# Kernel tuning notes

Measured on AMD Instinct MI355X. Metric: run time of the kernel, lower is better.

## Reference

```python
import jax, jax.numpy as jnp
import numpy as np

MAX_DISP = 192

def _conv(x, w, b=None, stride=1, pad=0):
    y = jax.lax.conv_general_dilated(x, w, (stride, stride), [(pad, pad), (pad, pad)],
                                     dimension_numbers=('NCHW', 'OIHW', 'NCHW'))
    return y if b is None else y + b[None, :, None, None]

def _inorm(x):  # InstanceNorm2d, affine=False
    m = x.mean((2, 3), keepdims=True)
    v = x.var((2, 3), keepdims=True)
    return (x - m) * jax.lax.rsqrt(v + 1e-5)

def _bnorm(x):  # BatchNorm2d at init (gamma=1, beta=0), batch stats
    m = x.mean((0, 2, 3), keepdims=True)
    v = x.var((0, 2, 3), keepdims=True)
    return (x - m) * jax.lax.rsqrt(v + 1e-5)

def _encoder(x, w1, b1, w2, b2, w3, b3, norm):
    # simplified BasicEncoder: two stride-2 convs -> 1/4 resolution, then 1x1 proj
    x = jax.nn.relu(norm(_conv(x, w1, b1, 2, 3)))
    x = jax.nn.relu(norm(_conv(x, w2, b2, 2, 1)))
    return _conv(x, w3, b3, 1, 0)

def _forward(image1, image2, fnet_w1, fnet_b1, fnet_w2, fnet_b2, fnet_w3, fnet_b3,
             cnet_w1, cnet_b1, cnet_w2, cnet_b2, cnet_w3, cnet_b3,
             bform_a, bform_b, bform_cd_w, bform_cd_b,
             gru_wz, gru_bz, gru_wr, gru_br, gru_wq, gru_bq,
             disp_w1, disp_b1, disp_w2, disp_b2):
    i1 = 2.0 * (image1 / 255.0) - 1.0
    i2 = 2.0 * (image2 / 255.0) - 1.0
    fmap1 = _encoder(i1, fnet_w1, fnet_b1, fnet_w2, fnet_b2, fnet_w3, fnet_b3, _inorm)
    fmap2 = _encoder(i2, fnet_w1, fnet_b1, fnet_w2, fnet_b2, fnet_w3, fnet_b3, _inorm)
    hidden = jnp.tanh(_encoder(i1, cnet_w1, cnet_b1, cnet_w2, cnet_b2, cnet_w3, cnet_b3, _bnorm))
    Wf = fmap1.shape[3]
    for d in range(MAX_DISP // 4):  # 48 sequential width-sweep steps, shrinking overlap
        f1 = fmap1[:, :, :, d:]
        f2 = fmap2[:, :, :, :Wf - d] if d > 0 else fmap2
        # BilinearForm: a(x) + b(y) + cd(x*y), all 1x1 convs
        feat = _conv(f1, bform_a) + _conv(f2, bform_b) + _conv(f1 * f2, bform_cd_w, bform_cd_b)
        h = hidden[:, :, :, d:]
        # gru_input = cat(h, feat); ConvGRU cats hidden again -> [h, h, feat] = 96 ch
        hx = jnp.concatenate([h, h, feat], axis=1)
        z = jax.nn.sigmoid(_conv(hx, gru_wz, gru_bz, 1, 1))
        r = jax.nn.sigmoid(_conv(hx, gru_wr, gru_br, 1, 1))
        q = jnp.tanh(_conv(jnp.concatenate([r * h, h, feat], axis=1), gru_wq, gru_bq, 1, 1))
        h = (1.0 - z) * h + z * q
        hidden = hidden.at[:, :, :, d:].set(h)  # in-place scatter back
    # DisparityHead: conv3x3 -> relu -> conv3x3, negated
    return -_conv(jax.nn.relu(_conv(hidden, disp_w1, disp_b1, 1, 1)), disp_w2, disp_b2, 1, 1)

def setup_inputs():
    key = jax.random.key(0)
    ks = jax.random.split(key, 16)
    B, H, W, D = 1, 384, 640, 32
    def n(k, shape, scale=0.05):
        return (jax.random.normal(k, shape) * scale).astype(jnp.float32)
    z = lambda c: jnp.zeros((c,), jnp.float32)
    return {
        'image1': jax.random.uniform(ks[0], (B, 3, H, W), jnp.float32) * 255.0,
        'image2': jax.random.uniform(ks[1], (B, 3, H, W), jnp.float32) * 255.0,
        'fnet_w1': n(ks[2], (D, 3, 7, 7)), 'fnet_b1': z(D),
        'fnet_w2': n(ks[3], (D, D, 3, 3)), 'fnet_b2': z(D),
        'fnet_w3': n(ks[4], (D, D, 1, 1)), 'fnet_b3': z(D),
        'cnet_w1': n(ks[5], (D, 3, 7, 7)), 'cnet_b1': z(D),
        'cnet_w2': n(ks[6], (D, D, 3, 3)), 'cnet_b2': z(D),
        'cnet_w3': n(ks[7], (D, D, 1, 1)), 'cnet_b3': z(D),
        'bform_a': n(ks[8], (D, D, 1, 1)), 'bform_b': n(ks[9], (D, D, 1, 1)),
        'bform_cd_w': n(ks[10], (D, D, 1, 1)), 'bform_cd_b': z(D),
        'gru_wz': n(ks[11], (D, 3 * D, 3, 3)), 'gru_bz': z(D),
        'gru_wr': n(ks[12], (D, 3 * D, 3, 3)), 'gru_br': z(D),
        'gru_wq': n(ks[13], (D, 3 * D, 3, 3)), 'gru_bq': z(D),
        'disp_w1': n(ks[14], (64, D, 3, 3)), 'disp_b1': z(64),
        'disp_w2': n(ks[15], (1, 64, 3, 3)), 'disp_b2': z(1),
    }

def reference(image1, image2, fnet_w1, fnet_b1, fnet_w2, fnet_b2, fnet_w3, fnet_b3,
              cnet_w1, cnet_b1, cnet_w2, cnet_b2, cnet_w3, cnet_b3,
              bform_a, bform_b, bform_cd_w, bform_cd_b,
              gru_wz, gru_bz, gru_wr, gru_br, gru_wq, gru_bq,
              disp_w1, disp_b1, disp_w2, disp_b2):
    return _forward(image1, image2, fnet_w1, fnet_b1, fnet_w2, fnet_b2, fnet_w3, fnet_b3,
                    cnet_w1, cnet_b1, cnet_w2, cnet_b2, cnet_w3, cnet_b3,
                    bform_a, bform_b, bform_cd_w, bform_cd_b,
                    gru_wz, gru_bz, gru_wr, gru_br, gru_wq, gru_bq,
                    disp_w1, disp_b1, disp_w2, disp_b2)
```

## Files before the change

kernel.cpp:

```cpp
#include <hip/hip_runtime.h>
#include <math.h>

#define H0 384
#define W0 640
#define H1 192
#define W1 320
#define H2 96
#define W2 160
#define NP1 (H1*W1)
#define NP2 (H2*W2)
#define ND  48
#define NBLK2 (NP2/256)
#define CHW ((size_t)32*NP2)
#define PW 162
#define PH 98
#define PSL (PH*PW)
#define PCHW ((size_t)32*PSL)

typedef float v2f __attribute__((ext_vector_type(2)));


__global__ void zero_buf_kernel(float* __restrict__ p, size_t n) {
    size_t i = (size_t)blockIdx.x*256 + threadIdx.x;
    size_t stride = (size_t)gridDim.x*256;
    for (; i < n; i += stride) p[i] = 0.f;
}

__device__ __forceinline__ void twr_dev(const float* __restrict__ in, float* __restrict__ out,
                                        int idx, int CI, int K, int CO) {
    int co = idx % CO;
    int t  = idx / CO;
    int k  = t % K;
    int ci = t / K;
    out[idx] = in[(co*CI + ci)*K + k];
}

__global__ void prep_all(const float* __restrict__ fnet_w1, const float* __restrict__ cnet_w1,
                         const float* __restrict__ fnet_w2, const float* __restrict__ cnet_w2,
                         const float* __restrict__ fnet_w3, const float* __restrict__ cnet_w3,
                         const float* __restrict__ bform_a, const float* __restrict__ bform_b,
                         const float* __restrict__ bform_cd_w, const float* __restrict__ disp_w1,
                         const float* __restrict__ gru_wz, const float* __restrict__ gru_wr,
                         const float* __restrict__ gru_wq,
                         float* __restrict__ we1f, float* __restrict__ we1c,
                         float* __restrict__ we2f, float* __restrict__ we2c,
                         float* __restrict__ w3f, float* __restrict__ w3c,
                         float* __restrict__ wat, float* __restrict__ wbt,
                         float* __restrict__ wct, float* __restrict__ wd1t,
                         float4* __restrict__ wzrpk, float2* __restrict__ wqpk,
                         float* __restrict__ stats) {
    int i = blockIdx.x*256 + threadIdx.x;
    if (i < 4704) { twr_dev(fnet_w1, we1f, i, 3, 49, 32); return; }
    i -= 4704;
    if (i < 4704) { twr_dev(cnet_w1, we1c, i, 3, 49, 32); return; }
    i -= 4704;
    if (i < 9216) { twr_dev(fnet_w2, we2f, i, 32, 9, 32); return; }
    i -= 9216;
    if (i < 9216) { twr_dev(cnet_w2, we2c, i, 32, 9, 32); return; }
    i -= 9216;
    if (i < 1024) { twr_dev(fnet_w3, w3f, i, 32, 1, 32); return; }
    i -= 1024;
    if (i < 1024) { twr_dev(cnet_w3, w3c, i, 32, 1, 32); return; }
    i -= 1024;
    if (i < 1024) { twr_dev(bform_a, wat, i, 32, 1, 32); return; }
    i -= 1024;
    if (i < 1024) { twr_dev(bform_b, wbt, i, 32, 1, 32); return; }
    i -= 1024;
    if (i < 1024) { twr_dev(bform_cd_w, wct, i, 32, 1, 32); return; }
    i -= 1024;
    if (i < 18432) { twr_dev(disp_w1, wd1t, i, 32, 9, 64); return; }
    i -= 18432;
    if (i < 9216) {
        int k  = i % 9;
        int ci = (i/9) % 64;
        int cg = i / (9*64);
        int co0 = cg*2, co1 = co0 + 1;
        float z0, z1, r0, r1;
        if (ci < 32) {
            z0 = gru_wz[(co0*96 + ci)*9 + k] + gru_wz[(co0*96 + ci + 32)*9 + k];
            z1 = gru_wz[(co1*96 + ci)*9 + k] + gru_wz[(co1*96 + ci + 32)*9 + k];
            r0 = gru_wr[(co0*96 + ci)*9 + k] + gru_wr[(co0*96 + ci + 32)*9 + k];
            r1 = gru_wr[(co1*96 + ci)*9 + k] + gru_wr[(co1*96 + ci + 32)*9 + k];
        } else {
            z0 = gru_wz[(co0*96 + ci + 32)*9 + k];
            z1 = gru_wz[(co1*96 + ci + 32)*9 + k];
            r0 = gru_wr[(co0*96 + ci + 32)*9 + k];
            r1 = gru_wr[(co1*96 + ci + 32)*9 + k];
        }
        wzrpk[i] = make_float4(z0, z1, r0, r1);
        return;
    }
    i -= 9216;
    if (i < 13824) {
        int k  = i % 9;
        int ci = (i/9) % 96;
        int cg = i / (9*96);
        wqpk[i] = make_float2(gru_wq[((cg*2)*96 + ci)*9 + k], gru_wq[((cg*2+1)*96 + ci)*9 + k]);
        return;
    }
    i -= 13824;
    if (i < 384) stats[i] = 0.f;
}

__global__ void pad_init_kernel(const float* __restrict__ hidden, float* __restrict__ hwork) {
    int idx = blockIdx.x*256 + threadIdx.x;
    if (idx >= 32*PSL) return;
    int c = idx / PSL;
    int r = idx % PSL;
    int py = r / PW, px = r % PW;
    int y = py - 1, x = px - 1;
    float v = 0.f;
    if ((unsigned)y < (unsigned)H2 && (unsigned)x < (unsigned)W2)
        v = hidden[c*NP2 + y*W2 + x];
    hwork[idx] = v;
}


__global__ __launch_bounds__(256, 4)
void conv7s2_dual(const float* __restrict__ img,
                  const float* __restrict__ wtf, const float* __restrict__ wtc,
                  const float* __restrict__ bf, const float* __restrict__ bc,
                  float* __restrict__ outf, float* __restrict__ outc) {
    int co8 = blockIdx.y*8;
    int sp = blockIdx.x*256 + threadIdx.x;
    int oy = sp / W1, ox = sp % W1;
    float af[8], ac[8];
    #pragma unroll
    for (int j = 0; j < 8; ++j) { af[j] = bf[co8+j]; ac[j] = bc[co8+j]; }
    for (int ci = 0; ci < 3; ++ci) {
        for (int ky = 0; ky < 7; ++ky) {
            int iy = 2*oy - 3 + ky;
            if ((unsigned)iy >= (unsigned)H0) continue;
            const float* row  = img + ci*(H0*W0) + iy*W0;
            int wbase = (ci*49 + ky*7)*32 + co8;
            #pragma unroll
            for (int kx = 0; kx < 7; ++kx) {
                int ix = 2*ox - 3 + kx;
                if ((unsigned)ix >= (unsigned)W0) continue;
                float v = row[ix]*(2.0f/255.0f) - 1.0f;
                const float4* wpf = (const float4*)(wtf + wbase + kx*32);
                const float4* wpc = (const float4*)(wtc + wbase + kx*32);
                float4 f0 = wpf[0], f1 = wpf[1];
                float4 c0 = wpc[0], c1 = wpc[1];
                af[0] += v*f0.x; af[1] += v*f0.y; af[2] += v*f0.z; af[3] += v*f0.w;
                af[4] += v*f1.x; af[5] += v*f1.y; af[6] += v*f1.z; af[7] += v*f1.w;
                ac[0] += v*c0.x; ac[1] += v*c0.y; ac[2] += v*c0.z; ac[3] += v*c0.w;
                ac[4] += v*c1.x; ac[5] += v*c1.y; ac[6] += v*c1.z; ac[7] += v*c1.w;
            }
        }
    }
    #pragma unroll
    for (int j = 0; j < 8; ++j) {
        outf[(co8+j)*NP1 + sp] = af[j];
        outc[(co8+j)*NP1 + sp] = ac[j];
    }
}

__global__ void conv7s2_v3(const float* __restrict__ img, const float* __restrict__ wt,
                           const float* __restrict__ b, float* __restrict__ out) {
    int cg = blockIdx.y;
    int co16 = cg*16;
    int sp = blockIdx.x*256 + threadIdx.x;
    int oy = sp / W1, ox = sp % W1;
    float acc[16];
    #pragma unroll
    for (int j = 0; j < 16; ++j) acc[j] = b[co16+j];
    for (int ci = 0; ci < 3; ++ci) {
        for (int ky = 0; ky < 7; ++ky) {
            int iy = 2*oy - 3 + ky;
            if ((unsigned)iy >= (unsigned)H0) continue;
            const float* row  = img + ci*(H0*W0) + iy*W0;
            const float* wrow = wt + (ci*49 + ky*7)*32 + co16;
            #pragma unroll
            for (int kx = 0; kx < 7; ++kx) {
                int ix = 2*ox - 3 + kx;
                if ((unsigned)ix >= (unsigned)W0) continue;
                float v = row[ix]*(2.0f/255.0f) - 1.0f;
                const float4* wp = (const float4*)(wrow + kx*32);
                #pragma unroll
                for (int j4 = 0; j4 < 4; ++j4) {
                    float4 w4 = wp[j4];
                    acc[4*j4+0] += v*w4.x; acc[4*j4+1] += v*w4.y;
                    acc[4*j4+2] += v*w4.z; acc[4*j4+3] += v*w4.w;
                }
            }
        }
    }
    #pragma unroll
    for (int j = 0; j < 16; ++j) out[(co16+j)*NP1 + sp] = acc[j];
}

__global__ void stats_partial_kernel(const float* __restrict__ x, int N, float* __restrict__ st) {
    int c = blockIdx.x >> 3, sl = blockIdx.x & 7;
    int chunk = N >> 3;
    const float4* p = (const float4*)(x + (size_t)c*N + (size_t)sl*chunk);
    int n4 = chunk >> 2;
    float s = 0.f, s2 = 0.f;
    for (int i = threadIdx.x; i < n4; i += 256) {
        float4 v = p[i];
        s  += v.x + v.y + v.z + v.w;
        s2 += v.x*v.x + v.y*v.y + v.z*v.z + v.w*v.w;
    }
    __shared__ float sh1[256], sh2[256];
    sh1[threadIdx.x] = s; sh2[threadIdx.x] = s2;
    __syncthreads();
    for (int o = 128; o > 0; o >>= 1) {
        if (threadIdx.x < o) { sh1[threadIdx.x] += sh1[threadIdx.x+o]; sh2[threadIdx.x] += sh2[threadIdx.x+o]; }
        __syncthreads();
    }
    if (threadIdx.x == 0) { atomicAdd(&st[2*c], sh1[0]); atomicAdd(&st[2*c+1], sh2[0]); }
}

__global__ void conv3s2_fused(const float* __restrict__ in, const float* __restrict__ st,
                              const float* __restrict__ wt, const float* __restrict__ b,
                              float* __restrict__ out) {
    int cg = blockIdx.x / NBLK2;
    int sp = (blockIdx.x % NBLK2)*256 + threadIdx.x;
    int co8 = cg*8;
    int oy = sp / W2, ox = sp % W2;
    float acc[8];
    #pragma unroll
    for (int j = 0; j < 8; ++j) acc[j] = b[co8+j];
    for (int ci = 0; ci < 32; ++ci) {
        float m    = st[2*ci] * (1.0f/NP1);
        float var  = st[2*ci+1] * (1.0f/NP1) - m*m;
        float rstd = rsqrtf(var + 1e-5f);
        const float* ip  = in + ci*NP1;
        const float* wci = wt + ci*9*32 + co8;
        #pragma unroll
        for (int ky = 0; ky < 3; ++ky) {
            int iy = 2*oy - 1 + ky;
            if ((unsigned)iy >= (unsigned)H1) continue;
            const float* row = ip + iy*W1;
            #pragma unroll
            for (int kx = 0; kx < 3; ++kx) {
                int ix = 2*ox - 1 + kx;
                if ((unsigned)ix >= (unsigned)W1) continue;
                float t = fmaxf((row[ix] - m)*rstd, 0.f);
                const float4* wp = (const float4*)(wci + (ky*3+kx)*32);
                float4 w0 = wp[0], w1 = wp[1];
                acc[0] += t*w0.x; acc[1] += t*w0.y; acc[2] += t*w0.z; acc[3] += t*w0.w;
                acc[4] += t*w1.x; acc[5] += t*w1.y; acc[6] += t*w1.z; acc[7] += t*w1.w;
            }
        }
    }
    #pragma unroll
    for (int j = 0; j < 8; ++j) out[(co8+j)*NP2 + sp] = acc[j];
}

__global__ void conv1x1_fused(const float* __restrict__ in, const float* __restrict__ st,
                              const float* __restrict__ wt, const float* __restrict__ b,
                              float* __restrict__ out, int mode) {
    int cg = blockIdx.x / NBLK2;
    int sp = (blockIdx.x % NBLK2)*256 + threadIdx.x;
    int co8 = cg*8;
    float acc[8];
    #pragma unroll
    for (int j = 0; j < 8; ++j) acc[j] = b[co8+j];
    for (int ci = 0; ci < 32; ++ci) {
        float m    = st[2*ci] * (1.0f/NP2);
        float var  = st[2*ci+1] * (1.0f/NP2) - m*m;
        float rstd = rsqrtf(var + 1e-5f);
        float t = fmaxf((in[ci*NP2 + sp] - m)*rstd, 0.f);
        const float4* wp = (const float4*)(wt + ci*32 + co8);
        float4 w0 = wp[0], w1 = wp[1];
        acc[0] += t*w0.x; acc[1] += t*w0.y; acc[2] += t*w0.z; acc[3] += t*w0.w;
        acc[4] += t*w1.x; acc[5] += t*w1.y; acc[6] += t*w1.z; acc[7] += t*w1.w;
    }
    #pragma unroll
    for (int j = 0; j < 8; ++j) {
        float a = acc[j];
        if (mode) a = tanhf(a);
        out[(co8+j)*NP2 + sp] = a;
    }
}


__global__ void feat0_pad_kernel(const float* __restrict__ fmap1, const float* __restrict__ fmap2,
                                 const float* __restrict__ wat, const float* __restrict__ wbt,
                                 const float* __restrict__ wct, const float* __restrict__ bc,
                                 float* __restrict__ featA) {
    int cg  = blockIdx.x / NBLK2;
    int sp  = (blockIdx.x % NBLK2)*256 + threadIdx.x;
    int y = sp / W2;
    int gx = sp % W2;
    int co8 = cg*8;
    float acc[8];
    #pragma unroll
    for (int j = 0; j < 8; ++j) acc[j] = bc[co8+j];
    for (int ci = 0; ci < 32; ++ci) {
        float f1 = fmap1[ci*NP2 + sp];
        float f2 = fmap2[ci*NP2 + sp];
        float f12 = f1*f2;
        const float4* ap = (const float4*)(wat + ci*32 + co8);
        const float4* bp = (const float4*)(wbt + ci*32 + co8);
        const float4* cp = (const float4*)(wct + ci*32 + co8);
        float4 a0 = ap[0], a1 = ap[1];
        float4 b0 = bp[0], b1 = bp[1];
        float4 c0 = cp[0], c1 = cp[1];
        acc[0] += f1*a0.x + f2*b0.x + f12*c0.x;
        acc[1] += f1*a0.y + f2*b0.y + f12*c0.y;
        acc[2] += f1*a0.z + f2*b0.z + f12*c0.z;
        acc[3] += f1*a0.w + f2*b0.w + f12*c0.w;
        acc[4] += f1*a1.x + f2*b1.x + f12*c1.x;
        acc[5] += f1*a1.y + f2*b1.y + f12*c1.y;
        acc[6] += f1*a1.z + f2*b1.z + f12*c1.z;
        acc[7] += f1*a1.w + f2*b1.w + f12*c1.w;
    }
    float* dst = featA + (size_t)(y+1)*PW + (gx+1);
    #pragma unroll
    for (int j = 0; j < 8; ++j) dst[(size_t)(co8+j)*PSL] = acc[j];
}


__global__ __launch_bounds__(256, 4)
void zrq_a(const float* __restrict__ hworkA, const float* __restrict__ featA,
           const float* __restrict__ fmap1, const float* __restrict__ fmap2,
           const float4* __restrict__ wzrpk, const float2* __restrict__ wqpk,
           const float* __restrict__ wat, const float* __restrict__ wbt,
           const float* __restrict__ wct, const float* __restrict__ bfc,
           const float* __restrict__ bz, const float* __restrict__ br,
           float* __restrict__ zbuf, float* __restrict__ rhpad,
           float* __restrict__ featB, float* __restrict__ qpart,
           int d, int Wd) {
    __shared__ v2f lws[1152];
    __shared__ v2f lfa[32], lfb[32], lfc[32];
    int cg  = blockIdx.y >> 1;
    int job = blockIdx.y & 1;
    int co0 = cg*2;
    if (job == 0) {
        const float4* wsrc = wzrpk + (size_t)cg*576;
        for (int i = threadIdx.x; i < 576; i += 256) {
            float4 w = wsrc[i];
            lws[i]       = (v2f){w.x, w.y};
            lws[576 + i] = (v2f){w.z, w.w};
        }
    } else {
        const float2* wsrc = wqpk + (size_t)cg*864 + 288;
        for (int i = threadIdx.x; i < 576; i += 256) {
            float2 w = wsrc[i];
            lws[i] = (v2f){w.x, w.y};
        }
        if (threadIdx.x < 32) {
            int ci = threadIdx.x;
            lfa[ci] = (v2f){wat[ci*32+co0], wat[ci*32+co0+1]};
            lfb[ci] = (v2f){wbt[ci*32+co0], wbt[ci*32+co0+1]};
            lfc[ci] = (v2f){wct[ci*32+co0], wct[ci*32+co0+1]};
        }
    }
    __syncthreads();
    int sp2 = blockIdx.x*256 + threadIdx.x;
    if (sp2 >= 48*Wd) return;
    int rp = sp2 / Wd;
    int lx = sp2 - rp*Wd;
    int y0 = rp*2;
    int gx = d + lx;
    size_t poff = (size_t)(y0+1)*PW + (gx+1);
    int ub = y0*W2 + gx;

    if (job == 0) {
        if (lx == 0) {
            #pragma unroll
            for (int j = 0; j < 2; ++j) {
                rhpad[(size_t)(co0+j)*PSL + poff - 1]      = 0.f;
                rhpad[(size_t)(co0+j)*PSL + poff + PW - 1] = 0.f;
            }
        }
        v2f az0 = (v2f){bz[co0], bz[co0+1]}, az1 = az0;
        v2f ar0 = (v2f){br[co0], br[co0+1]}, ar1 = ar0;
        #pragma unroll
        for (int pass = 0; pass < 2; ++pass) {
            const float* p = (pass == 0 ? hworkA : featA) + poff;
            const v2f* wz = lws + pass*288;
            const v2f* wr = lws + 576 + pass*288;
            #pragma unroll 2
            for (int ci = 0; ci < 32; ++ci) {
                float v[12];
                #pragma unroll
                for (int r = 0; r < 4; ++r) {
                    v[r*3+0] = p[(r-1)*PW - 1];
                    v[r*3+1] = p[(r-1)*PW    ];
                    v[r*3+2] = p[(r-1)*PW + 1];
                }
                #pragma unroll
                for (int k = 0; k < 9; ++k) {
                    int ky = k/3, kx = k - 3*ky;
                    float t0 = v[ky*3+kx];
                    float t1 = v[(ky+1)*3+kx];
                    v2f wzk = wz[k], wrk = wr[k];
                    az0 += wzk*(v2f){t0,t0}; az1 += wzk*(v2f){t1,t1};
                    ar0 += wrk*(v2f){t0,t0}; ar1 += wrk*(v2f){t1,t1};
                }
                p += PSL;
                wz += 9; wr += 9;
            }
        }
        v2f z0, z1, r0, r1;
        z0.x = 1.f/(1.f + __expf(-az0.x)); z0.y = 1.f/(1.f + __expf(-az0.y));
        z1.x = 1.f/(1.f + __expf(-az1.x)); z1.y = 1.f/(1.f + __expf(-az1.y));
        r0.x = 1.f/(1.f + __expf(-ar0.x)); r0.y = 1.f/(1.f + __expf(-ar0.y));
        r1.x = 1.f/(1.f + __expf(-ar1.x)); r1.y = 1.f/(1.f + __expf(-ar1.y));
        float h00 = hworkA[(size_t)co0*PSL + poff];
        float h01 = hworkA[(size_t)(co0+1)*PSL + poff];
        float h10 = hworkA[(size_t)co0*PSL + poff + PW];
        float h11 = hworkA[(size_t)(co0+1)*PSL + poff + PW];
        zbuf[(size_t)co0*NP2 + ub]          = z0.x;
        zbuf[(size_t)(co0+1)*NP2 + ub]      = z0.y;
        zbuf[(size_t)co0*NP2 + ub + W2]     = z1.x;
        zbuf[(size_t)(co0+1)*NP2 + ub + W2] = z1.y;
        rhpad[(size_t)co0*PSL + poff]          = r0.x*h00;
        rhpad[(size_t)(co0+1)*PSL + poff]      = r0.y*h01;
        rhpad[(size_t)co0*PSL + poff + PW]     = r1.x*h10;
        rhpad[(size_t)(co0+1)*PSL + poff + PW] = r1.y*h11;
    } else {
        int dn = d + 1;
        if (dn < ND) {
            if (lx == 0) {
                #pragma unroll
                for (int j = 0; j < 2; ++j) {
                    featB[(size_t)(co0+j)*PSL + poff]      = 0.f;
                    featB[(size_t)(co0+j)*PSL + poff + PW] = 0.f;
                }
            } else {
                v2f f0 = (v2f){bfc[co0], bfc[co0+1]};
                v2f f1 = f0;
                int base1 = y0*W2 + gx;
                #pragma unroll 2
                for (int ci = 0; ci < 32; ++ci) {
                    float a1 = fmap1[ci*NP2 + base1];
                    float a2 = fmap1[ci*NP2 + base1 + W2];
                    float b1 = fmap2[ci*NP2 + base1 - dn];
                    float b2 = fmap2[ci*NP2 + base1 + W2 - dn];
                    v2f wa = lfa[ci], wb = lfb[ci], wc = lfc[ci];
                    f0 += wa*(v2f){a1,a1} + wb*(v2f){b1,b1} + wc*(v2f){a1*b1,a1*b1};
                    f1 += wa*(v2f){a2,a2} + wb*(v2f){b2,b2} + wc*(v2f){a2*b2,a2*b2};
                }
                featB[(size_t)co0*PSL + poff]          = f0.x;
                featB[(size_t)(co0+1)*PSL + poff]      = f0.y;
                featB[(size_t)co0*PSL + poff + PW]     = f1.x;
                featB[(size_t)(co0+1)*PSL + poff + PW] = f1.y;
            }
        }
        v2f a0 = (v2f){0.f, 0.f};
        v2f a1 = a0;
        #pragma unroll
        for (int pass = 0; pass < 2; ++pass) {
            const float* p = (pass == 0 ? hworkA : featA) + poff;
            const v2f* wp = lws + pass*288;
            #pragma unroll 2
            for (int ci = 0; ci < 32; ++ci) {
                float v[12];
                #pragma unroll
                for (int r = 0; r < 4; ++r) {
                    v[r*3+0] = p[(r-1)*PW - 1];
                    v[r*3+1] = p[(r-1)*PW    ];
                    v[r*3+2] = p[(r-1)*PW + 1];
                }
                #pragma unroll
                for (int k = 0; k < 9; ++k) {
                    int ky = k/3, kx = k - 3*ky;
                    float t0 = v[ky*3+kx];
                    float t1 = v[(ky+1)*3+kx];
                    v2f wk = wp[k];
                    a0 += wk*(v2f){t0,t0};
                    a1 += wk*(v2f){t1,t1};
                }
                p += PSL;
                wp += 9;
            }
        }
        qpart[(size_t)co0*NP2 + ub]          = a0.x;
        qpart[(size_t)(co0+1)*NP2 + ub]      = a0.y;
        qpart[(size_t)co0*NP2 + ub + W2]     = a1.x;
        qpart[(size_t)(co0+1)*NP2 + ub + W2] = a1.y;
    }
}

__global__ __launch_bounds__(256, 4)
void q_fin(const float* __restrict__ rhpad, const float* __restrict__ hworkA,
           const float* __restrict__ zbuf, const float* __restrict__ qpart,
           const float2* __restrict__ wqpk, const float* __restrict__ bq,
           float* __restrict__ hfinal, float* __restrict__ hworkB, int d, int Wd) {
    __shared__ v2f lw[288];
    int cg  = blockIdx.y;
    int co0 = cg*2;
    {
        const float2* wsrc = wqpk + (size_t)cg*864;
        for (int i = threadIdx.x; i < 288; i += 256) {
            float2 w = wsrc[i];
            lw[i] = (v2f){w.x, w.y};
        }
    }
    __syncthreads();
    int sp2 = blockIdx.x*256 + threadIdx.x;
    if (sp2 >= 48*Wd) return;
    int rp = sp2 / Wd;
    int lx = sp2 - rp*Wd;
    int y0 = rp*2;
    int gx = d + lx;
    size_t poff = (size_t)(y0+1)*PW + (gx+1);
    int ub = y0*W2 + gx;

    v2f a0 = (v2f){bq[co0], bq[co0+1]};
    v2f a1 = a0;
    {
        const float* p = rhpad + poff;
        const v2f* wp = lw;
        #pragma unroll 2
        for (int ci = 0; ci < 32; ++ci) {
            float v[12];
            #pragma unroll
            for (int r = 0; r < 4; ++r) {
                v[r*3+0] = p[(r-1)*PW - 1];
                v[r*3+1] = p[(r-1)*PW    ];
                v[r*3+2] = p[(r-1)*PW + 1];
            }
            #pragma unroll
            for (int k = 0; k < 9; ++k) {
                int ky = k/3, kx = k - 3*ky;
                float t0 = v[ky*3+kx];
                float t1 = v[(ky+1)*3+kx];
                v2f wk = wp[k];
                a0 += wk*(v2f){t0,t0};
                a1 += wk*(v2f){t1,t1};
            }
            p += PSL;
            wp += 9;
        }
    }
    a0.x += qpart[(size_t)co0*NP2 + ub];
    a0.y += qpart[(size_t)(co0+1)*NP2 + ub];
    a1.x += qpart[(size_t)co0*NP2 + ub + W2];
    a1.y += qpart[(size_t)(co0+1)*NP2 + ub + W2];
    float q00 = tanhf(a0.x), q01 = tanhf(a0.y);
    float q10 = tanhf(a1.x), q11 = tanhf(a1.y);
    #pragma unroll
    for (int j = 0; j < 2; ++j) {
        float qa = (j == 0) ? q00 : q01;
        float qb = (j == 0) ? q10 : q11;
        size_t pidx = (size_t)(co0+j)*PSL + poff;
        size_t uidx = (size_t)(co0+j)*NP2 + ub;
        float z_a = zbuf[uidx];
        float z_b = zbuf[uidx + W2];
        float h_a = hworkA[pidx];
        float h_b = hworkA[pidx + PW];
        float hn_a = (1.f - z_a)*h_a + z_a*qa;
        float hn_b = (1.f - z_b)*h_b + z_b*qb;
        if (lx == 0 || d == ND-1) {
            hfinal[pidx]      = hn_a;
            hfinal[pidx + PW] = hn_b;
        }
        hworkB[pidx]      = (lx == 0) ? 0.f : hn_a;
        hworkB[pidx + PW] = (lx == 0) ? 0.f : hn_b;
    }
}


__global__ __launch_bounds__(256, 4)
void disp1_v6(const float* __restrict__ hfinal, const float* __restrict__ wt,
              const float* __restrict__ b, float* __restrict__ out) {
    __shared__ float4 lw[288];
    int cg  = blockIdx.y;
    int co0 = cg*4;
    for (int i = threadIdx.x; i < 288; i += 256)
        lw[i] = *(const float4*)&wt[i*64 + co0];
    __syncthreads();
    int sp2 = blockIdx.x*256 + threadIdx.x;
    int y0 = (sp2 / W2)*2;
    int gx = sp2 % W2;
    size_t poff = (size_t)(y0+1)*PW + (gx+1);
    float4 bb = *(const float4*)&b[co0];
    float acc0[4] = {bb.x, bb.y, bb.z, bb.w};
    float acc1[4] = {bb.x, bb.y, bb.z, bb.w};
    const float* p = hfinal + poff;
    #pragma unroll 2
    for (int ci = 0; ci < 32; ++ci) {
        float v[12];
        #pragma unroll
        for (int r = 0; r < 4; ++r) {
            v[r*3+0] = p[(r-1)*PW - 1];
            v[r*3+1] = p[(r-1)*PW    ];
            v[r*3+2] = p[(r-1)*PW + 1];
        }
        #pragma unroll
        for (int k = 0; k < 9; ++k) {
            int ky = k/3, kx = k - 3*ky;
            float t0 = v[ky*3+kx];
            float t1 = v[(ky+1)*3+kx];
            float4 w = lw[ci*9+k];
            acc0[0] += t0*w.x; acc0[1] += t0*w.y; acc0[2] += t0*w.z; acc0[3] += t0*w.w;
            acc1[0] += t1*w.x; acc1[1] += t1*w.y; acc1[2] += t1*w.z; acc1[3] += t1*w.w;
        }
        p += PSL;
    }
    int ub = y0*W2 + gx;
    #pragma unroll
    for (int j = 0; j < 4; ++j) {
        out[(co0+j)*NP2 + ub]      = fmaxf(acc0[j], 0.f);
        out[(co0+j)*NP2 + ub + W2] = fmaxf(acc1[j], 0.f);
    }
}

__global__ void disp2_part_kernel(const float* __restrict__ in, const float* __restrict__ w,
                                  float* __restrict__ part) {
    __shared__ float lw[8*9];
    int g  = blockIdx.x / NBLK2;
    int sp = (blockIdx.x % NBLK2)*256 + threadIdx.x;
    if (threadIdx.x < 72) lw[threadIdx.x] = w[g*72 + threadIdx.x];
    __syncthreads();
    int y = sp / W2, x = sp % W2;
    float acc = 0.f;
    #pragma unroll
    for (int ci = 0; ci < 8; ++ci) {
        const float* ip = in + (g*8 + ci)*NP2;
        #pragma unroll
        for (int dy = 0; dy < 3; ++dy) {
            int ys = y+dy-1; if ((unsigned)ys >= (unsigned)H2) continue;
            const float* row = ip + ys*W2;
            #pragma unroll
            for (int dx = 0; dx < 3; ++dx) {
                int xs = x+dx-1; if ((unsigned)xs >= (unsigned)W2) continue;
                acc += lw[ci*9+dy*3+dx] * row[xs];
            }
        }
    }
    part[g*NP2 + sp] = acc;
}

__global__ void disp2_comb_kernel(const float* __restrict__ part, const float* __restrict__ b,
                                  float* __restrict__ out) {
    int sp = blockIdx.x*256 + threadIdx.x;
    float acc = b[0];
    #pragma unroll
    for (int g = 0; g < 8; ++g) acc += part[g*NP2 + sp];
    out[sp] = -acc;
}


extern "C" void kernel_launch(void* const* d_in, const int* in_sizes, int n_in,
                              void* d_out, int out_size, void* d_ws, size_t ws_size,
                              hipStream_t stream) {
    const float* image1   = (const float*)d_in[0];
    const float* image2   = (const float*)d_in[1];
    const float* fnet_w1  = (const float*)d_in[2];
    const float* fnet_b1  = (const float*)d_in[3];
    const float* fnet_w2  = (const float*)d_in[4];
    const float* fnet_b2  = (const float*)d_in[5];
    const float* fnet_w3  = (const float*)d_in[6];
    const float* fnet_b3  = (const float*)d_in[7];
    const float* cnet_w1  = (const float*)d_in[8];
    const float* cnet_b1  = (const float*)d_in[9];
    const float* cnet_w2  = (const float*)d_in[10];
    const float* cnet_b2  = (const float*)d_in[11];
    const float* cnet_w3  = (const float*)d_in[12];
    const float* cnet_b3  = (const float*)d_in[13];
    const float* bform_a  = (const float*)d_in[14];
    const float* bform_b  = (const float*)d_in[15];
    const float* bform_cd_w = (const float*)d_in[16];
    const float* bform_cd_b = (const float*)d_in[17];
    const float* gru_wz   = (const float*)d_in[18];
    const float* gru_bz   = (const float*)d_in[19];
    const float* gru_wr   = (const float*)d_in[20];
    const float* gru_br   = (const float*)d_in[21];
    const float* gru_wq   = (const float*)d_in[22];
    const float* gru_bq   = (const float*)d_in[23];
    const float* disp_w1  = (const float*)d_in[24];
    const float* disp_b1  = (const float*)d_in[25];
    const float* disp_w2  = (const float*)d_in[26];
    const float* disp_b2  = (const float*)d_in[27];

    float* ws = (float*)d_ws;
    size_t o = 0;
    float* e1f    = ws + o; o += (size_t)32*NP1;
    float* e1c    = ws + o; o += (size_t)32*NP1;
    float* e2     = ws + o; o += CHW;
    float* fmap1  = ws + o; o += CHW;
    float* fmap2  = ws + o; o += CHW;
    float* hidden = ws + o; o += CHW;
    float* zbuf   = ws + o; o += CHW;
    float* qpart  = ws + o; o += CHW;
    float* hwork0 = ws + o; o += PCHW;
    float* hwork1 = ws + o; o += PCHW;
    float* rhpad  = ws + o; o += PCHW;
    float* feat0  = ws + o; o += PCHW;
    float* feat1  = ws + o; o += PCHW;
    float* hfinal = ws + o; o += PCHW;
    float* stats  = ws + o; o += 384;
    float* wzrpk  = ws + o; o += 16*64*9*4;
    float* wqpk   = ws + o; o += 16*96*9*2;
    float* we1f   = ws + o; o += 3*49*32;
    float* we1c   = ws + o; o += 3*49*32;
    float* we2f   = ws + o; o += 32*9*32;
    float* we2c   = ws + o; o += 32*9*32;
    float* w3f    = ws + o; o += 32*32;
    float* w3c    = ws + o; o += 32*32;
    float* wat    = ws + o; o += 32*32;
    float* wbt    = ws + o; o += 32*32;
    float* wct    = ws + o; o += 32*32;
    float* wd1t   = ws + o; o += 32*9*64;
    float* disp1buf  = e1f;
    float* disp2part = e1c;

    prep_all<<<(74816 + 255)/256, 256, 0, stream>>>(
        fnet_w1, cnet_w1, fnet_w2, cnet_w2, fnet_w3, cnet_w3,
        bform_a, bform_b, bform_cd_w, disp_w1, gru_wz, gru_wr, gru_wq,
        we1f, we1c, we2f, we2c, w3f, w3c, wat, wbt, wct, wd1t,
        (float4*)wzrpk, (float2*)wqpk, stats);

    conv7s2_dual<<<dim3(NP1/256, 4), 256, 0, stream>>>(image1, we1f, we1c, fnet_b1, cnet_b1,
                                                       e1f, e1c);
    stats_partial_kernel<<<256, 256, 0, stream>>>(e1f, NP1, stats+0);
    stats_partial_kernel<<<256, 256, 0, stream>>>(e1c, NP1, stats+64);
    conv3s2_fused<<<4*NBLK2, 256, 0, stream>>>(e1f, stats+0, we2f, fnet_b2, e2);
    stats_partial_kernel<<<256, 256, 0, stream>>>(e2, NP2, stats+128);
    conv1x1_fused<<<4*NBLK2, 256, 0, stream>>>(e2, stats+128, w3f, fnet_b3, fmap1, 0);
    conv3s2_fused<<<4*NBLK2, 256, 0, stream>>>(e1c, stats+64, we2c, cnet_b2, e2);
    stats_partial_kernel<<<256, 256, 0, stream>>>(e2, NP2, stats+192);
    conv1x1_fused<<<4*NBLK2, 256, 0, stream>>>(e2, stats+192, w3c, cnet_b3, hidden, 1);
    conv7s2_v3<<<dim3(NP1/256, 2), 256, 0, stream>>>(image2, we1f, fnet_b1, e1f);
    stats_partial_kernel<<<256, 256, 0, stream>>>(e1f, NP1, stats+256);
    conv3s2_fused<<<4*NBLK2, 256, 0, stream>>>(e1f, stats+256, we2f, fnet_b2, e2);
    stats_partial_kernel<<<256, 256, 0, stream>>>(e2, NP2, stats+320);
    conv1x1_fused<<<4*NBLK2, 256, 0, stream>>>(e2, stats+320, w3f, fnet_b3, fmap2, 0);

    zero_buf_kernel<<<2048, 256, 0, stream>>>(hwork1, 5*PCHW);
    pad_init_kernel<<<(32*PSL+255)/256, 256, 0, stream>>>(hidden, hwork0);
    feat0_pad_kernel<<<4*NBLK2, 256, 0, stream>>>(fmap1, fmap2, wat, wbt, wct,
                                                  bform_cd_b, feat0);

    float* hwA = hwork0; float* hwB = hwork1;
    float* ftA = feat0;  float* ftB = feat1;
    for (int d = 0; d < ND; ++d) {
        int Wd = W2 - d;
        int nblk = (48*Wd + 255)/256;
        zrq_a<<<dim3(nblk, 32), 256, 0, stream>>>(hwA, ftA, fmap1, fmap2,
                                                  (const float4*)wzrpk, (const float2*)wqpk,
                                                  wat, wbt, wct, bform_cd_b,
                                                  gru_bz, gru_br, zbuf, rhpad, ftB, qpart,
                                                  d, Wd);
        q_fin<<<dim3(nblk, 16), 256, 0, stream>>>(rhpad, hwA, zbuf, qpart,
                                                  (const float2*)wqpk, gru_bq,
                                                  hfinal, hwB, d, Wd);
        float* t;
        t = hwA; hwA = hwB; hwB = t;
        t = ftA; ftA = ftB; ftB = t;
    }

    disp1_v6<<<dim3(30, 16), 256, 0, stream>>>(hfinal, wd1t, disp_b1, disp1buf);
    disp2_part_kernel<<<8*NBLK2, 256, 0, stream>>>(disp1buf, disp_w2, disp2part);
    disp2_comb_kernel<<<NBLK2, 256, 0, stream>>>(disp2part, disp_b2, (float*)d_out);
}
```

Before: 2.681 ms.

## Fuse norm statistics into conv epilogues and split q-partial job across more blocks

Removes the separate stats_partial reduction kernels by having each conv kernel reduce its outputs per wavefront with shuffles and atomically add channel sum and sum-of-squares. It also splits the zrq_a q-partial work (hidden pass and feat pass) into two separate block jobs writing to two buffers, raising the grid from 32 to 48 y-blocks, and q_fin sums both partials. This trades extra atomics and an extra buffer read for fewer launches, less re-reading of activations, and more parallelism in the per-step loop. Atomic accumulation order changes floating-point summation order slightly.

Result: slower. 4.017 ms (+49.8%).

```diff
diff --git a/kernel.cpp b/kernel.cpp
--- a/kernel.cpp
+++ b/kernel.cpp
@@ -18,6 +18,24 @@
 #define PCHW ((size_t)32*PSL)
 
 typedef float v2f __attribute__((ext_vector_type(2)));
+
+__device__ __forceinline__ void wave_stats(float* __restrict__ st, int ch0,
+                                           const float* acc, int n) {
+    int lane = threadIdx.x & 63;
+    for (int j = 0; j < n; ++j) {
+        float s  = acc[j];
+        float s2 = s*s;
+        #pragma unroll
+        for (int off = 32; off > 0; off >>= 1) {
+            s  += __shfl_down(s,  off, 64);
+            s2 += __shfl_down(s2, off, 64);
+        }
+        if (lane == 0) {
+            atomicAdd(&st[2*(ch0+j)],   s);
+            atomicAdd(&st[2*(ch0+j)+1], s2);
+        }
+    }
+}
 
 
 __global__ void zero_buf_kernel(float* __restrict__ p, size_t n) {
@@ -120,7 +138,8 @@
 void conv7s2_dual(const float* __restrict__ img,
                   const float* __restrict__ wtf, const float* __restrict__ wtc,
                   const float* __restrict__ bf, const float* __restrict__ bc,
-                  float* __restrict__ outf, float* __restrict__ outc) {
+                  float* __restrict__ outf, float* __restrict__ outc,
+                  float* __restrict__ stf, float* __restrict__ stc) {
     int co8 = blockIdx.y*8;
     int sp = blockIdx.x*256 + threadIdx.x;
     int oy = sp / W1, ox = sp % W1;
@@ -154,10 +173,13 @@
         outf[(co8+j)*NP1 + sp] = af[j];
         outc[(co8+j)*NP1 + sp] = ac[j];
     }
+    wave_stats(stf, co8, af, 8);
+    wave_stats(stc, co8, ac, 8);
 }
 
 __global__ void conv7s2_v3(const float* __restrict__ img, const float* __restrict__ wt,
-                           const float* __restrict__ b, float* __restrict__ out) {
+                           const float* __restrict__ b, float* __restrict__ out,
+                           float* __restrict__ st) {
     int cg = blockIdx.y;
     int co16 = cg*16;
     int sp = blockIdx.x*256 + threadIdx.x;
@@ -188,32 +210,12 @@
     }
     #pragma unroll
     for (int j = 0; j < 16; ++j) out[(co16+j)*NP1 + sp] = acc[j];
-}
-
-__global__ void stats_partial_kernel(const float* __restrict__ x, int N, float* __restrict__ st) {
-    int c = blockIdx.x >> 3, sl = blockIdx.x & 7;
-    int chunk = N >> 3;
-    const float4* p = (const float4*)(x + (size_t)c*N + (size_t)sl*chunk);
-    int n4 = chunk >> 2;
-    float s = 0.f, s2 = 0.f;
-    for (int i = threadIdx.x; i < n4; i += 256) {
-        float4 v = p[i];
-        s  += v.x + v.y + v.z + v.w;
-        s2 += v.x*v.x + v.y*v.y + v.z*v.z + v.w*v.w;
-    }
-    __shared__ float sh1[256], sh2[256];
-    sh1[threadIdx.x] = s; sh2[threadIdx.x] = s2;
-    __syncthreads();
-    for (int o = 128; o > 0; o >>= 1) {
-        if (threadIdx.x < o) { sh1[threadIdx.x] += sh1[threadIdx.x+o]; sh2[threadIdx.x] += sh2[threadIdx.x+o]; }
-        __syncthreads();
-    }
-    if (threadIdx.x == 0) { atomicAdd(&st[2*c], sh1[0]); atomicAdd(&st[2*c+1], sh2[0]); }
+    wave_stats(st, co16, acc, 16);
 }
 
 __global__ void conv3s2_fused(const float* __restrict__ in, const float* __restrict__ st,
                               const float* __restrict__ wt, const float* __restrict__ b,
-                              float* __restrict__ out) {
+                              float* __restrict__ out, float* __restrict__ stout) {
     int cg = blockIdx.x / NBLK2;
     int sp = (blockIdx.x % NBLK2)*256 + threadIdx.x;
     int co8 = cg*8;
@@ -246,6 +248,7 @@
     }
     #pragma unroll
     for (int j = 0; j < 8; ++j) out[(co8+j)*NP2 + sp] = acc[j];
+    wave_stats(stout, co8, acc, 8);
 }
 
 __global__ void conv1x1_fused(const float* __restrict__ in, const float* __restrict__ st,
@@ -321,12 +324,12 @@
            const float* __restrict__ wct, const float* __restrict__ bfc,
            const float* __restrict__ bz, const float* __restrict__ br,
            float* __restrict__ zbuf, float* __restrict__ rhpad,
-           float* __restrict__ featB, float* __restrict__ qpart,
-           int d, int Wd) {
+           float* __restrict__ featB, float* __restrict__ qpartA,
+           float* __restrict__ qpartB, int d, int Wd) {
     __shared__ v2f lws[1152];
     __shared__ v2f lfa[32], lfb[32], lfc[32];
-    int cg  = blockIdx.y >> 1;
-    int job = blockIdx.y & 1;
+    int cg  = blockIdx.y / 3;
+    int job = blockIdx.y - cg*3;
     int co0 = cg*2;
     if (job == 0) {
         const float4* wsrc = wzrpk + (size_t)cg*576;
@@ -335,9 +338,9 @@
             lws[i]       = (v2f){w.x, w.y};
             lws[576 + i] = (v2f){w.z, w.w};
         }
-    } else {
+    } else if (job == 1) {
         const float2* wsrc = wqpk + (size_t)cg*864 + 288;
-        for (int i = threadIdx.x; i < 576; i += 256) {
+        for (int i = threadIdx.x; i < 288; i += 256) {
             float2 w = wsrc[i];
             lws[i] = (v2f){w.x, w.y};
         }
@@ -346,6 +349,12 @@
             lfa[ci] = (v2f){wat[ci*32+co0], wat[ci*32+co0+1]};
             lfb[ci] = (v2f){wbt[ci*32+co0], wbt[ci*32+co0+1]};
             lfc[ci] = (v2f){wct[ci*32+co0], wct[ci*32+co0+1]};
+        }
+    } else {
+        const float2* wsrc = wqpk + (size_t)cg*864 + 576;
+        for (int i = threadIdx.x; i < 288; i += 256) {
+            float2 w = wsrc[i];
+            lws[i] = (v2f){w.x, w.y};
         }
     }
     __syncthreads();
@@ -412,7 +421,7 @@
         rhpad[(size_t)(co0+1)*PSL + poff]      = r0.y*h01;
         rhpad[(size_t)co0*PSL + poff + PW]     = r1.x*h10;
         rhpad[(size_t)(co0+1)*PSL + poff + PW] = r1.y*h11;
-    } else {
+    } else if (job == 1) {
         int dn = d + 1;
         if (dn < ND) {
             if (lx == 0) {
@@ -443,10 +452,9 @@
         }
         v2f a0 = (v2f){0.f, 0.f};
         v2f a1 = a0;
-        #pragma unroll
-        for (int pass = 0; pass < 2; ++pass) {
-            const float* p = (pass == 0 ? hworkA : featA) + poff;
-            const v2f* wp = lws + pass*288;
+        {
+            const float* p = hworkA + poff;
+            const v2f* wp = lws;
             #pragma unroll 2
             for (int ci = 0; ci < 32; ++ci) {
                 float v[12];
@@ -469,16 +477,49 @@
                 wp += 9;
             }
         }
-        qpart[(size_t)co0*NP2 + ub]          = a0.x;
-        qpart[(size_t)(co0+1)*NP2 + ub]      = a0.y;
-        qpart[(size_t)co0*NP2 + ub + W2]     = a1.x;
-        qpart[(size_t)(co0+1)*NP2 + ub + W2] = a1.y;
+        qpartA[(size_t)co0*NP2 + ub]          = a0.x;
+        qpartA[(size_t)(co0+1)*NP2 + ub]      = a0.y;
+        qpartA[(size_t)co0*NP2 + ub + W2]     = a1.x;
+        qpartA[(size_t)(co0+1)*NP2 + ub + W2] = a1.y;
+    } else {
+        v2f a0 = (v2f){0.f, 0.f};
+        v2f a1 = a0;
+        {
+            const float* p = featA + poff;
+            const v2f* wp = lws;
+            #pragma unroll 2
+            for (int ci = 0; ci < 32; ++ci) {
+                float v[12];
+                #pragma unroll
+                for (int r = 0; r < 4; ++r) {
+                    v[r*3+0] = p[(r-1)*PW - 1];
+                    v[r*3+1] = p[(r-1)*PW    ];
+                    v[r*3+2] = p[(r-1)*PW + 1];
+                }
+                #pragma unroll
+                for (int k = 0; k < 9; ++k) {
+                    int ky = k/3, kx = k - 3*ky;
+                    float t0 = v[ky*3+kx];
+                    float t1 = v[(ky+1)*3+kx];
+                    v2f wk = wp[k];
+                    a0 += wk*(v2f){t0,t0};
+                    a1 += wk*(v2f){t1,t1};
+                }
+                p += PSL;
+                wp += 9;
+            }
+        }
+        qpartB[(size_t)co0*NP2 + ub]          = a0.x;
+        qpartB[(size_t)(co0+1)*NP2 + ub]      = a0.y;
+        qpartB[(size_t)co0*NP2 + ub + W2]     = a1.x;
+        qpartB[(size_t)(co0+1)*NP2 + ub + W2] = a1.y;
     }
 }
 
 __global__ __launch_bounds__(256, 4)
 void q_fin(const float* __restrict__ rhpad, const float* __restrict__ hworkA,
-           const float* __restrict__ zbuf, const float* __restrict__ qpart,
+           const float* __restrict__ zbuf, const float* __restrict__ qpartA,
+           const float* __restrict__ qpartB,
            const float2* __restrict__ wqpk, const float* __restrict__ bq,
            float* __restrict__ hfinal, float* __restrict__ hworkB, int d, int Wd) {
     __shared__ v2f lw[288];
@@ -520,7 +561,7 @@
                 int ky = k/3, kx = k - 3*ky;
                 float t0 = v[ky*3+kx];
                 float t1 = v[(ky+1)*3+kx];
-                v2f wk = wp[k];
+                v2f wk = lw[(wp - lw) + k];
                 a0 += wk*(v2f){t0,t0};
                 a1 += wk*(v2f){t1,t1};
             }
@@ -528,10 +569,10 @@
             wp += 9;
         }
     }
-    a0.x += qpart[(size_t)co0*NP2 + ub];
-    a0.y += qpart[(size_t)(co0+1)*NP2 + ub];
-    a1.x += qpart[(size_t)co0*NP2 + ub + W2];
-    a1.y += qpart[(size_t)(co0+1)*NP2 + ub + W2];
+    a0.x += qpartA[(size_t)co0*NP2 + ub]          + qpartB[(size_t)co0*NP2 + ub];
+    a0.y += qpartA[(size_t)(co0+1)*NP2 + ub]      + qpartB[(size_t)(co0+1)*NP2 + ub];
+    a1.x += qpartA[(size_t)co0*NP2 + ub + W2]     + qpartB[(size_t)co0*NP2 + ub + W2];
+    a1.y += qpartA[(size_t)(co0+1)*NP2 + ub + W2] + qpartB[(size_t)(co0+1)*NP2 + ub + W2];
     float q00 = tanhf(a0.x), q01 = tanhf(a0.y);
     float q10 = tanhf(a1.x), q11 = tanhf(a1.y);
     #pragma unroll
@@ -678,7 +719,8 @@
     float* fmap2  = ws + o; o += CHW;
     float* hidden = ws + o; o += CHW;
     float* zbuf   = ws + o; o += CHW;
-    float* qpart  = ws + o; o += CHW;
+    float* qpartA = ws + o; o += CHW;
+    float* qpartB = ws + o; o += CHW;
     float* hwork0 = ws + o; o += PCHW;
     float* hwork1 = ws + o; o += PCHW;
     float* rhpad  = ws + o; o += PCHW;
@@ -708,19 +750,13 @@
         (float4*)wzrpk, (float2*)wqpk, stats);
 
     conv7s2_dual<<<dim3(NP1/256, 4), 256, 0, stream>>>(image1, we1f, we1c, fnet_b1, cnet_b1,
-                                                       e1f, e1c);
-    stats_partial_kernel<<<256, 256, 0, stream>>>(e1f, NP1, stats+0);
-    stats_partial_kernel<<<256, 256, 0, stream>>>(e1c, NP1, stats+64);
-    conv3s2_fused<<<4*NBLK2, 256, 0, stream>>>(e1f, stats+0, we2f, fnet_b2, e2);
-    stats_partial_kernel<<<256, 256, 0, stream>>>(e2, NP2, stats+128);
+                                                       e1f, e1c, stats+0, stats+64);
+    conv3s2_fused<<<4*NBLK2, 256, 0, stream>>>(e1f, stats+0, we2f, fnet_b2, e2, stats+128);
     conv1x1_fused<<<4*NBLK2, 256, 0, stream>>>(e2, stats+128, w3f, fnet_b3, fmap1, 0);
-    conv3s2_fused<<<4*NBLK2, 256, 0, stream>>>(e1c, stats+64, we2c, cnet_b2, e2);
-    stats_partial_kernel<<<256, 256, 0, stream>>>(e2, NP2, stats+192);
+    conv3s2_fused<<<4*NBLK2, 256, 0, stream>>>(e1c, stats+64, we2c, cnet_b2, e2, stats+192);
     conv1x1_fused<<<4*NBLK2, 256, 0, stream>>>(e2, stats+192, w3c, cnet_b3, hidden, 1);
-    conv7s2_v3<<<dim3(NP1/256, 2), 256, 0, stream>>>(image2, we1f, fnet_b1, e1f);
-    stats_partial_kernel<<<256, 256, 0, stream>>>(e1f, NP1, stats+256);
-    conv3s2_fused<<<4*NBLK2, 256, 0, stream>>>(e1f, stats+256, we2f, fnet_b2, e2);
-    stats_partial_kernel<<<256, 256, 0, stream>>>(e2, NP2, stats+320);
+    conv7s2_v3<<<dim3(NP1/256, 2), 256, 0, stream>>>(image2, we1f, fnet_b1, e1f, stats+256);
+    conv3s2_fused<<<4*NBLK2, 256, 0, stream>>>(e1f, stats+256, we2f, fnet_b2, e2, stats+320);
     conv1x1_fused<<<4*NBLK2, 256, 0, stream>>>(e2, stats+320, w3f, fnet_b3, fmap2, 0);
 
     zero_buf_kernel<<<2048, 256, 0, stream>>>(hwork1, 5*PCHW);
@@ -733,12 +769,12 @@
     for (int d = 0; d < ND; ++d) {
         int Wd = W2 - d;
         int nblk = (48*Wd + 255)/256;
-        zrq_a<<<dim3(nblk, 32), 256, 0, stream>>>(hwA, ftA, fmap1, fmap2,
+        zrq_a<<<dim3(nblk, 48), 256, 0, stream>>>(hwA, ftA, fmap1, fmap2,
                                                   (const float4*)wzrpk, (const float2*)wqpk,
                                                   wat, wbt, wct, bform_cd_b,
-                                                  gru_bz, gru_br, zbuf, rhpad, ftB, qpart,
-                                                  d, Wd);
-        q_fin<<<dim3(nblk, 16), 256, 0, stream>>>(rhpad, hwA, zbuf, qpart,
+                                                  gru_bz, gru_br, zbuf, rhpad, ftB,
+                                                  qpartA, qpartB, d, Wd);
+        q_fin<<<dim3(nblk, 16), 256, 0, stream>>>(rhpad, hwA, zbuf, qpartA, qpartB,
                                                   (const float2*)wqpk, gru_bq,
                                                   hfinal, hwB, d, Wd);
         float* t;
```

## Batch the three encoder passes into single launches per stage

Applied to the files above, without the earlier changes.

Merges the fnet(image1), cnet(image1) and fnet(image2) encoder pipelines so that each stage (7x7 conv, stats, 3x3 conv, stats, 1x1 conv) runs as one grid that covers all three networks. This takes the encoder from 14 launches down to 5 and gives each launch more blocks, which should fill the GPU better during the small encoder stages. The 7x7 conv now uses 8 output channels per thread with launch_bounds raised to 8 blocks per SM. Separate intermediate buffers are allocated for each net, which uses more workspace. The encoder is probably a small share of the total time next to the 48-step GRU loop.

Result: faster. 2.554 ms (-4.7%).

```diff
diff --git a/kernel.cpp b/kernel.cpp
--- a/kernel.cpp
+++ b/kernel.cpp
@@ -116,81 +116,51 @@
 }
 
 
-__global__ __launch_bounds__(256, 4)
-void conv7s2_dual(const float* __restrict__ img,
-                  const float* __restrict__ wtf, const float* __restrict__ wtc,
-                  const float* __restrict__ bf, const float* __restrict__ bc,
-                  float* __restrict__ outf, float* __restrict__ outc) {
-    int co8 = blockIdx.y*8;
+__global__ __launch_bounds__(256, 8)
+void conv7s2_all(const float* __restrict__ img1, const float* __restrict__ img2,
+                 const float* __restrict__ wtf, const float* __restrict__ wtc,
+                 const float* __restrict__ bf, const float* __restrict__ bc,
+                 float* __restrict__ e1f, float* __restrict__ e1c, float* __restrict__ e1i2) {
+    int net = blockIdx.y >> 2;
+    int co8 = (blockIdx.y & 3)*8;
+    const float* img = (net == 2) ? img2 : img1;
+    const float* wt  = (net == 1) ? wtc : wtf;
+    const float* bb  = (net == 1) ? bc  : bf;
+    float* out = (net == 0) ? e1f : (net == 1 ? e1c : e1i2);
     int sp = blockIdx.x*256 + threadIdx.x;
     int oy = sp / W1, ox = sp % W1;
-    float af[8], ac[8];
-    #pragma unroll
-    for (int j = 0; j < 8; ++j) { af[j] = bf[co8+j]; ac[j] = bc[co8+j]; }
+    float acc[8];
+    #pragma unroll
+    for (int j = 0; j < 8; ++j) acc[j] = bb[co8+j];
     for (int ci = 0; ci < 3; ++ci) {
         for (int ky = 0; ky < 7; ++ky) {
             int iy = 2*oy - 3 + ky;
             if ((unsigned)iy >= (unsigned)H0) continue;
             const float* row  = img + ci*(H0*W0) + iy*W0;
-            int wbase = (ci*49 + ky*7)*32 + co8;
-            #pragma unroll
-            for (int kx = 0; kx < 7; ++kx) {
-                int ix = 2*ox - 3 + kx;
-                if ((unsigned)ix >= (unsigned)W0) continue;
-                float v = row[ix]*(2.0f/255.0f) - 1.0f;
-                const float4* wpf = (const float4*)(wtf + wbase + kx*32);
-                const float4* wpc = (const float4*)(wtc + wbase + kx*32);
-                float4 f0 = wpf[0], f1 = wpf[1];
-                float4 c0 = wpc[0], c1 = wpc[1];
-                af[0] += v*f0.x; af[1] += v*f0.y; af[2] += v*f0.z; af[3] += v*f0.w;
-                af[4] += v*f1.x; af[5] += v*f1.y; af[6] += v*f1.z; af[7] += v*f1.w;
-                ac[0] += v*c0.x; ac[1] += v*c0.y; ac[2] += v*c0.z; ac[3] += v*c0.w;
-                ac[4] += v*c1.x; ac[5] += v*c1.y; ac[6] += v*c1.z; ac[7] += v*c1.w;
-            }
-        }
-    }
-    #pragma unroll
-    for (int j = 0; j < 8; ++j) {
-        outf[(co8+j)*NP1 + sp] = af[j];
-        outc[(co8+j)*NP1 + sp] = ac[j];
-    }
-}
-
-__global__ void conv7s2_v3(const float* __restrict__ img, const float* __restrict__ wt,
-                           const float* __restrict__ b, float* __restrict__ out) {
-    int cg = blockIdx.y;
-    int co16 = cg*16;
-    int sp = blockIdx.x*256 + threadIdx.x;
-    int oy = sp / W1, ox = sp % W1;
-    float acc[16];
-    #pragma unroll
-    for (int j = 0; j < 16; ++j) acc[j] = b[co16+j];
-    for (int ci = 0; ci < 3; ++ci) {
-        for (int ky = 0; ky < 7; ++ky) {
-            int iy = 2*oy - 3 + ky;
-            if ((unsigned)iy >= (unsigned)H0) continue;
-            const float* row  = img + ci*(H0*W0) + iy*W0;
-            const float* wrow = wt + (ci*49 + ky*7)*32 + co16;
+            const float* wrow = wt + (ci*49 + ky*7)*32 + co8;
             #pragma unroll
             for (int kx = 0; kx < 7; ++kx) {
                 int ix = 2*ox - 3 + kx;
                 if ((unsigned)ix >= (unsigned)W0) continue;
                 float v = row[ix]*(2.0f/255.0f) - 1.0f;
                 const float4* wp = (const float4*)(wrow + kx*32);
-                #pragma unroll
-                for (int j4 = 0; j4 < 4; ++j4) {
-                    float4 w4 = wp[j4];
-                    acc[4*j4+0] += v*w4.x; acc[4*j4+1] += v*w4.y;
-                    acc[4*j4+2] += v*w4.z; acc[4*j4+3] += v*w4.w;
-                }
-            }
-        }
-    }
-    #pragma unroll
-    for (int j = 0; j < 16; ++j) out[(co16+j)*NP1 + sp] = acc[j];
-}
-
-__global__ void stats_partial_kernel(const float* __restrict__ x, int N, float* __restrict__ st) {
+                float4 w0 = wp[0], w1 = wp[1];
+                acc[0] += v*w0.x; acc[1] += v*w0.y; acc[2] += v*w0.z; acc[3] += v*w0.w;
+                acc[4] += v*w1.x; acc[5] += v*w1.y; acc[6] += v*w1.z; acc[7] += v*w1.w;
+            }
+        }
+    }
+    #pragma unroll
+    for (int j = 0; j < 8; ++j) out[(co8+j)*NP1 + sp] = acc[j];
+}
+
+__global__ void stats3_kernel(const float* __restrict__ b0, const float* __restrict__ b1,
+                              const float* __restrict__ b2, int N,
+                              float* __restrict__ st0, float* __restrict__ st1,
+                              float* __restrict__ st2) {
+    int job = blockIdx.y;
+    const float* x = (job == 0) ? b0 : (job == 1 ? b1 : b2);
+    float* st      = (job == 0) ? st0 : (job == 1 ? st1 : st2);
     int c = blockIdx.x >> 3, sl = blockIdx.x & 7;
     int chunk = N >> 3;
     const float4* p = (const float4*)(x + (size_t)c*N + (size_t)sl*chunk);
@@ -211,12 +181,20 @@
     if (threadIdx.x == 0) { atomicAdd(&st[2*c], sh1[0]); atomicAdd(&st[2*c+1], sh2[0]); }
 }
 
-__global__ void conv3s2_fused(const float* __restrict__ in, const float* __restrict__ st,
-                              const float* __restrict__ wt, const float* __restrict__ b,
-                              float* __restrict__ out) {
-    int cg = blockIdx.x / NBLK2;
-    int sp = (blockIdx.x % NBLK2)*256 + threadIdx.x;
-    int co8 = cg*8;
+__global__ void conv3s2_all(const float* __restrict__ e1f, const float* __restrict__ e1c,
+                            const float* __restrict__ e1i2, const float* __restrict__ stats,
+                            const float* __restrict__ we2f, const float* __restrict__ we2c,
+                            const float* __restrict__ fb2, const float* __restrict__ cb2,
+                            float* __restrict__ e2f, float* __restrict__ e2c,
+                            float* __restrict__ e2i2) {
+    int net = blockIdx.y >> 2;
+    int co8 = (blockIdx.y & 3)*8;
+    const float* in = (net == 0) ? e1f : (net == 1 ? e1c : e1i2);
+    const float* st = (net == 0) ? stats+0 : (net == 1 ? stats+64 : stats+256);
+    const float* wt = (net == 1) ? we2c : we2f;
+    const float* b  = (net == 1) ? cb2 : fb2;
+    float* out = (net == 0) ? e2f : (net == 1 ? e2c : e2i2);
+    int sp = blockIdx.x*256 + threadIdx.x;
     int oy = sp / W2, ox = sp % W2;
     float acc[8];
     #pragma unroll
@@ -248,12 +226,20 @@
     for (int j = 0; j < 8; ++j) out[(co8+j)*NP2 + sp] = acc[j];
 }
 
-__global__ void conv1x1_fused(const float* __restrict__ in, const float* __restrict__ st,
-                              const float* __restrict__ wt, const float* __restrict__ b,
-                              float* __restrict__ out, int mode) {
-    int cg = blockIdx.x / NBLK2;
-    int sp = (blockIdx.x % NBLK2)*256 + threadIdx.x;
-    int co8 = cg*8;
+__global__ void conv1x1_all(const float* __restrict__ e2f, const float* __restrict__ e2c,
+                            const float* __restrict__ e2i2, const float* __restrict__ stats,
+                            const float* __restrict__ w3f, const float* __restrict__ w3c,
+                            const float* __restrict__ fb3, const float* __restrict__ cb3,
+                            float* __restrict__ fmap1, float* __restrict__ hiddenb,
+                            float* __restrict__ fmap2) {
+    int net = blockIdx.y >> 2;
+    int co8 = (blockIdx.y & 3)*8;
+    const float* in = (net == 0) ? e2f : (net == 1 ? e2c : e2i2);
+    const float* st = (net == 0) ? stats+128 : (net == 1 ? stats+192 : stats+320);
+    const float* wt = (net == 1) ? w3c : w3f;
+    const float* b  = (net == 1) ? cb3 : fb3;
+    float* out = (net == 0) ? fmap1 : (net == 1 ? hiddenb : fmap2);
+    int sp = blockIdx.x*256 + threadIdx.x;
     float acc[8];
     #pragma unroll
     for (int j = 0; j < 8; ++j) acc[j] = b[co8+j];
@@ -270,7 +256,7 @@
     #pragma unroll
     for (int j = 0; j < 8; ++j) {
         float a = acc[j];
-        if (mode) a = tanhf(a);
+        if (net == 1) a = tanhf(a);
         out[(co8+j)*NP2 + sp] = a;
     }
 }
@@ -673,7 +659,10 @@
     size_t o = 0;
     float* e1f    = ws + o; o += (size_t)32*NP1;
     float* e1c    = ws + o; o += (size_t)32*NP1;
-    float* e2     = ws + o; o += CHW;
+    float* e1i2   = ws + o; o += (size_t)32*NP1;
+    float* e2f    = ws + o; o += CHW;
+    float* e2c    = ws + o; o += CHW;
+    float* e2i2   = ws + o; o += CHW;
     float* fmap1  = ws + o; o += CHW;
     float* fmap2  = ws + o; o += CHW;
     float* hidden = ws + o; o += CHW;
@@ -707,21 +696,18 @@
         we1f, we1c, we2f, we2c, w3f, w3c, wat, wbt, wct, wd1t,
         (float4*)wzrpk, (float2*)wqpk, stats);
 
-    conv7s2_dual<<<dim3(NP1/256, 4), 256, 0, stream>>>(image1, we1f, we1c, fnet_b1, cnet_b1,
-                                                       e1f, e1c);
-    stats_partial_kernel<<<256, 256, 0, stream>>>(e1f, NP1, stats+0);
-    stats_partial_kernel<<<256, 256, 0, stream>>>(e1c, NP1, stats+64);
-    conv3s2_fused<<<4*NBLK2, 256, 0, stream>>>(e1f, stats+0, we2f, fnet_b2, e2);
-    stats_partial_kernel<<<256, 256, 0, stream>>>(e2, NP2, stats+128);
-    conv1x1_fused<<<4*NBLK2, 256, 0, stream>>>(e2, stats+128, w3f, fnet_b3, fmap1, 0);
-    conv3s2_fused<<<4*NBLK2, 256, 0, stream>>>(e1c, stats+64, we2c, cnet_b2, e2);
-    stats_partial_kernel<<<256, 256, 0, stream>>>(e2, NP2, stats+192);
-    conv1x1_fused<<<4*NBLK2, 256, 0, stream>>>(e2, stats+192, w3c, cnet_b3, hidden, 1);
-    conv7s2_v3<<<dim3(NP1/256, 2), 256, 0, stream>>>(image2, we1f, fnet_b1, e1f);
-    stats_partial_kernel<<<256, 256, 0, stream>>>(e1f, NP1, stats+256);
-    conv3s2_fused<<<4*NBLK2, 256, 0, stream>>>(e1f, stats+256, we2f, fnet_b2, e2);
-    stats_partial_kernel<<<256, 256, 0, stream>>>(e2, NP2, stats+320);
-    conv1x1_fused<<<4*NBLK2, 256, 0, stream>>>(e2, stats+320, w3f, fnet_b3, fmap2, 0);
+    conv7s2_all<<<dim3(NP1/256, 12), 256, 0, stream>>>(image1, image2, we1f, we1c,
+                                                       fnet_b1, cnet_b1, e1f, e1c, e1i2);
+    stats3_kernel<<<dim3(256, 3), 256, 0, stream>>>(e1f, e1c, e1i2, NP1,
+                                                    stats+0, stats+64, stats+256);
+    conv3s2_all<<<dim3(NBLK2, 12), 256, 0, stream>>>(e1f, e1c, e1i2, stats,
+                                                     we2f, we2c, fnet_b2, cnet_b2,
+                                                     e2f, e2c, e2i2);
+    stats3_kernel<<<dim3(256, 3), 256, 0, stream>>>(e2f, e2c, e2i2, NP2,
+                                                    stats+128, stats+192, stats+320);
+    conv1x1_all<<<dim3(NBLK2, 12), 256, 0, stream>>>(e2f, e2c, e2i2, stats,
+                                                     w3f, w3c, fnet_b3, cnet_b3,
+                                                     fmap1, hidden, fmap2);
 
     zero_buf_kernel<<<2048, 256, 0, stream>>>(hwork1, 5*PCHW);
     pad_init_kernel<<<(32*PSL+255)/256, 256, 0, stream>>>(hidden, hwork0);
```
